# Kernel tuning notes

Measured on AMD Instinct MI355X. Metric: run time of the kernel, lower is better.

Reference implementation:

```python
import jax, jax.numpy as jnp
import numpy as np

N = 50000
E = 800000
T = 12
HID = 128
K = 3
F_IN = 7  # 1 (x) + 4 (env) + 2 (coords)
CIN = F_IN + HID  # DCRNN concatenates input with hidden state


def setup_inputs() -> dict:
    key = jax.random.key(0)
    ks = jax.random.split(key, 16)
    inp = {
        "x": jax.random.normal(ks[0], (N, T), dtype=jnp.float32),
        "env": jax.random.normal(ks[1], (N, 4, T), dtype=jnp.float32),
        "coords": jax.random.uniform(ks[2], (N, 2), dtype=jnp.float32),
        "edge_index": jax.random.randint(ks[3], (2, E), 0, N, dtype=jnp.int32),
        "edge_weight": jax.random.uniform(ks[4], (E,), dtype=jnp.float32),
        "local_night": jax.random.uniform(ks[5], (N, T + 1), dtype=jnp.float32),
        # DCRNN gate diffusion-conv weights: [2 (out/in direction), K, Cin, Cout]
        "Wz": jax.random.normal(ks[6], (2, K, CIN, HID), dtype=jnp.float32) * 0.05,
        "bz": jnp.zeros((HID,), dtype=jnp.float32),
        "Wr": jax.random.normal(ks[7], (2, K, CIN, HID), dtype=jnp.float32) * 0.05,
        "br": jnp.zeros((HID,), dtype=jnp.float32),
        "Wh": jax.random.normal(ks[8], (2, K, CIN, HID), dtype=jnp.float32) * 0.05,
        "bh": jnp.zeros((HID,), dtype=jnp.float32),
        "lin_W": jax.random.normal(ks[9], (HID, 1), dtype=jnp.float32) * 0.05,
        "lin_b": jnp.zeros((1,), dtype=jnp.float32),
    }
    return inp


def reference(x, env, coords, edge_weight, local_night, Wz, bz, Wr, br, Wh, bh, lin_W, lin_b, edge_index):
    row, col = edge_index[0], edge_index[1]
    n = x.shape[0]

    # out/in degrees of the weighted adjacency A[row, col] = w
    deg_out = jax.ops.segment_sum(edge_weight, row, num_segments=n)
    deg_in = jax.ops.segment_sum(edge_weight, col, num_segments=n)
    inv_out = jnp.where(deg_out > 0, 1.0 / deg_out, 0.0)
    inv_in = jnp.where(deg_in > 0, 1.0 / deg_in, 0.0)

    def prop_out(v):  # (D_O^{-1} A) v : gather from col, scatter-add to row
        msg = edge_weight[:, None] * v[col]
        return inv_out[:, None] * jax.ops.segment_sum(msg, row, num_segments=n)

    def prop_in(v):  # (D_I^{-1} A^T) v : gather from row, scatter-add to col
        msg = edge_weight[:, None] * v[row]
        return inv_in[:, None] * jax.ops.segment_sum(msg, col, num_segments=n)

    def dconv(X, W, b):
        # K-hop bidirectional diffusion convolution
        H = X @ (W[0, 0] + W[1, 0])
        Tx0 = X
        Tx_o = prop_out(X)
        Tx_i = prop_in(X)
        H = H + Tx_o @ W[0, 1] + Tx_i @ W[1, 1]
        for k in range(2, W.shape[1]):
            Tx_o = 2.0 * prop_out(Tx_o) - Tx0
            Tx_i = 2.0 * prop_in(Tx_i) - Tx0
            H = H + Tx_o @ W[0, k] + Tx_i @ W[1, k]
        return H + b

    env_t = jnp.moveaxis(env, -1, 0)          # [T, N, 4]
    night_t = jnp.transpose(local_night[:, 1:])  # [T, N]
    hid0 = jnp.zeros((n, HID), dtype=x.dtype)   # hidden state resets each call (H=None)

    def step(x_prev, ts):
        e, night = ts
        X = jnp.concatenate([x_prev, e, coords], axis=1)   # [N, 7]
        Xh = jnp.concatenate([X, hid0], axis=1)            # [N, 7+HID]
        Z = jax.nn.sigmoid(dconv(Xh, Wz, bz))
        R = jax.nn.sigmoid(dconv(Xh, Wr, br))  # H*R = 0 since H0 = 0; kept for fidelity
        H_tilde = jnp.tanh(dconv(Xh, Wh, bh))
        H_new = Z * hid0 + (1.0 - Z) * H_tilde
        out = jax.nn.relu(H_new) @ lin_W + lin_b           # [N, 1]
        out = out * night[:, None]
        return out, out

    x0 = x[:, 0:1]
    _, preds = jax.lax.scan(step, x0, (env_t, night_t))    # preds: [T, N, 1]
    predictions = jnp.concatenate([x0, jnp.transpose(preds[..., 0])], axis=1)  # [N, T+1]
    return predictions
```

## Files before the change

### kernel.cpp

```cpp
#include <hip/hip_runtime.h>
#include <hip/hip_fp16.h>

#define Nn 50000
#define Ee 800000
#define Tt 12
#define NBAND 8
#define BAND 6250
#define NSB 32
#define NCHUNKS ((Nn + NSB - 1) / NSB)
#define SCB 196

__global__ __launch_bounds__(256) void hist_kernel(
    const int* __restrict__ ei, int* __restrict__ cntR, int* __restrict__ cntC)
{
    int e = blockIdx.x * 256 + threadIdx.x;
    if (e >= Ee) return;
    atomicAdd(&cntR[ei[e]], 1);
    atomicAdd(&cntC[ei[Ee + e]], 1);
}

__global__ __launch_bounds__(256) void scanA_kernel(
    const int* __restrict__ cntR, const int* __restrict__ cntC,
    int* __restrict__ bsum)
{
    const int* cnt = blockIdx.y ? cntC : cntR;
    int i = blockIdx.x * 256 + threadIdx.x;
    int v = (i < Nn) ? cnt[i] : 0;
    __shared__ int ws_[4];
    v += __shfl_xor(v, 1);  v += __shfl_xor(v, 2);  v += __shfl_xor(v, 4);
    v += __shfl_xor(v, 8);  v += __shfl_xor(v, 16); v += __shfl_xor(v, 32);
    if ((threadIdx.x & 63) == 0) ws_[threadIdx.x >> 6] = v;
    __syncthreads();
    if (threadIdx.x == 0)
        bsum[blockIdx.y * 256 + blockIdx.x] = ws_[0] + ws_[1] + ws_[2] + ws_[3];
}

__global__ __launch_bounds__(256) void scanB_kernel(
    const int* __restrict__ bsum, int* __restrict__ bbase)
{
    int y = blockIdx.x;
    __shared__ int s[256];
    int t = threadIdx.x;
    int v = (t < SCB) ? bsum[y * 256 + t] : 0;
    s[t] = v;
    __syncthreads();
    for (int off = 1; off < 256; off <<= 1) {
        int u = (t >= off) ? s[t - off] : 0;
        __syncthreads();
        s[t] += u;
        __syncthreads();
    }
    bbase[y * 256 + t] = s[t] - v;
}

__global__ __launch_bounds__(256) void scanC_kernel(
    const int* __restrict__ cntR, const int* __restrict__ cntC,
    const int* __restrict__ bbase,
    int* __restrict__ startR, int* __restrict__ startC,
    int* __restrict__ nextR, int* __restrict__ nextC)
{
    int y = blockIdx.y;
    const int* cnt = y ? cntC : cntR;
    int* start     = y ? startC : startR;
    int* nxt       = y ? nextC : nextR;
    int i = blockIdx.x * 256 + threadIdx.x;
    int v = (i < Nn) ? cnt[i] : 0;
    __shared__ int s[256];
    int t = threadIdx.x;
    s[t] = v;
    __syncthreads();
    for (int off = 1; off < 256; off <<= 1) {
        int u = (t >= off) ? s[t - off] : 0;
        __syncthreads();
        s[t] += u;
        __syncthreads();
    }
    int st = bbase[y * 256 + blockIdx.x] + s[t] - v;
    if (i < Nn) { start[i] = st; nxt[i] = st; }
}

__global__ __launch_bounds__(256) void scatter_banded(
    const int* __restrict__ ei, const float* __restrict__ ew,
    int* __restrict__ nextR, int* __restrict__ nextC,
    unsigned* __restrict__ adjR, unsigned* __restrict__ adjC)
{
    int band = blockIdx.x & (NBAND - 1);
    int chunk = blockIdx.x >> 3;
    int lo = band * BAND, hi = lo + BAND;
    int stride = (gridDim.x >> 3) * 256;
    for (int e = chunk * 256 + threadIdx.x; e < Ee; e += stride) {
        int r = ei[e], c = ei[Ee + e];
        bool wr = (r >= lo && r < hi);
        bool wc = (c >= lo && c < hi);
        if (!(wr || wc)) continue;
        unsigned wb = __half_as_ushort(__float2half(ew[e]));
        if (wr) adjR[atomicAdd(&nextR[r], 1)] = ((unsigned)c << 16) | wb;
        if (wc) adjC[atomicAdd(&nextC[c], 1)] = ((unsigned)r << 16) | wb;
    }
}

__global__ __launch_bounds__(256) void weff_kernel(
    const float* __restrict__ Wz, const float* __restrict__ Wh,
    const float* __restrict__ bz, const float* __restrict__ bh,
    float* __restrict__ wzT, float* __restrict__ whT)
{
    int idx = blockIdx.x * 256 + threadIdx.x;
    if (idx >= 2 * 36 * 128) return;
    const float* W = (idx < 36 * 128) ? Wz : Wh;
    const float* B = (idx < 36 * 128) ? bz : bh;
    float* O       = (idx < 36 * 128) ? wzT : whT;
    int rem = idx % (36 * 128);
    int k = rem / 128, j = rem % 128;
    float v;
    if (k == 35) v = B[j];
    else {
        int p = k / 7, rr = k % 7;
        if (p == 0)      v = W[(0 * 135 + rr) * 128 + j] + W[(3 * 135 + rr) * 128 + j];
        else if (p == 1) v = W[(1 * 135 + rr) * 128 + j];
        else if (p == 2) v = W[(4 * 135 + rr) * 128 + j];
        else if (p == 3) v = W[(2 * 135 + rr) * 128 + j];
        else             v = W[(5 * 135 + rr) * 128 + j];
    }
    O[k * 128 + j] = v;
}

__global__ __launch_bounds__(256) void init_kernel(
    const float* __restrict__ x, const float* __restrict__ env,
    const float* __restrict__ coords, __half* __restrict__ Xh,
    float* __restrict__ out)
{
    int i = blockIdx.x * 256 + threadIdx.x;
    if (i >= Nn) return;
    float xv = x[i * Tt];
    __half* r = Xh + (long)i * 8;
    r[0] = __float2half(xv);
    #pragma unroll
    for (int c = 0; c < 4; c++) r[1 + c] = __float2half(env[i * 48 + c * 12]);
    r[5] = __float2half(coords[i * 2 + 0]);
    r[6] = __float2half(coords[i * 2 + 1]);
    r[7] = __half(0.f);
    out[i * 13 + 0] = xv;
}

__device__ __forceinline__ void unpack8(const __half* p, float* v) {
    uint4 hv = *((const uint4*)p);
    float2 p0 = __half22float2(*(__half2*)&hv.x);
    float2 p1 = __half22float2(*(__half2*)&hv.y);
    float2 p2 = __half22float2(*(__half2*)&hv.z);
    float2 p3 = __half22float2(*(__half2*)&hv.w);
    v[0] = p0.x; v[1] = p0.y; v[2] = p1.x; v[3] = p1.y;
    v[4] = p2.x; v[5] = p2.y; v[6] = p3.x;
}

__device__ __forceinline__ void pack8(__half* p, const float* v) {
    __half2 q0 = __floats2half2_rn(v[0], v[1]);
    __half2 q1 = __floats2half2_rn(v[2], v[3]);
    __half2 q2 = __floats2half2_rn(v[4], v[5]);
    __half2 q3 = __floats2half2_rn(v[6], 0.f);
    uint4 st;
    st.x = *(unsigned*)&q0; st.y = *(unsigned*)&q1;
    st.z = *(unsigned*)&q2; st.w = *(unsigned*)&q3;
    *((uint4*)p) = st;
}

__global__ __launch_bounds__(256) void gather1_kernel(
    const int* __restrict__ startR, const int* __restrict__ cntR,
    const unsigned* __restrict__ adjR,
    const int* __restrict__ startC, const int* __restrict__ cntC,
    const unsigned* __restrict__ adjC,
    const __half* __restrict__ Xh,
    __half* __restrict__ TxoH, __half* __restrict__ TxiH,
    float* __restrict__ inv_out, float* __restrict__ inv_in)
{
    int tid = blockIdx.x * 256 + threadIdx.x;
    if (tid >= Nn * 8) return;
    int node = tid >> 3;
    int dir = (tid >> 2) & 1, sub = tid & 3;
    const int*      st  = dir ? startC : startR;
    const int*      cn  = dir ? cntC : cntR;
    const unsigned* adj = dir ? adjC : adjR;
    int b = st[node], e = b + cn[node];
    float a[7] = {0.f, 0.f, 0.f, 0.f, 0.f, 0.f, 0.f};
    float sw = 0.f;
    for (int k = b + sub; k < e; k += 4) {
        unsigned ed = adj[k];
        float w = __half2float(__ushort_as_half((unsigned short)(ed & 0xffffu)));
        float xv[7];
        unpack8(Xh + (long)(ed >> 16) * 8, xv);
        #pragma unroll
        for (int q = 0; q < 7; q++) a[q] = fmaf(w, xv[q], a[q]);
        sw += w;
    }
    #pragma unroll
    for (int m = 1; m <= 2; m <<= 1) {
        #pragma unroll
        for (int q = 0; q < 7; q++) a[q] += __shfl_xor(a[q], m);
        sw += __shfl_xor(sw, m);
    }
    if (sub == 0) {
        float inv = sw > 0.f ? 1.f / sw : 0.f;
        (dir ? inv_in : inv_out)[node] = inv;
        #pragma unroll
        for (int q = 0; q < 7; q++) a[q] *= inv;
        pack8((dir ? TxiH : TxoH) + (long)node * 8, a);
    }
}

__global__ __launch_bounds__(256) void gather2_kernel(
    const int* __restrict__ startR, const int* __restrict__ cntR,
    const unsigned* __restrict__ adjR,
    const int* __restrict__ startC, const int* __restrict__ cntC,
    const unsigned* __restrict__ adjC,
    const __half* __restrict__ Xh,
    const __half* __restrict__ TxoH, const __half* __restrict__ TxiH,
    const float* __restrict__ inv_out, const float* __restrict__ inv_in,
    __half* __restrict__ T2oH, __half* __restrict__ T2iH)
{
    int tid = blockIdx.x * 256 + threadIdx.x;
    if (tid >= Nn * 8) return;
    int node = tid >> 3;
    int dir = (tid >> 2) & 1, sub = tid & 3;
    const int*      st  = dir ? startC : startR;
    const int*      cn  = dir ? cntC : cntR;
    const unsigned* adj = dir ? adjC : adjR;
    const __half*   src = dir ? TxiH : TxoH;
    int b = st[node], e = b + cn[node];
    float a[7] = {0.f, 0.f, 0.f, 0.f, 0.f, 0.f, 0.f};
    for (int k = b + sub; k < e; k += 4) {
        unsigned ed = adj[k];
        float w = __half2float(__ushort_as_half((unsigned short)(ed & 0xffffu)));
        float xv[7];
        unpack8(src + (long)(ed >> 16) * 8, xv);
        #pragma unroll
        for (int q = 0; q < 7; q++) a[q] = fmaf(w, xv[q], a[q]);
    }
    #pragma unroll
    for (int m = 1; m <= 2; m <<= 1) {
        #pragma unroll
        for (int q = 0; q < 7; q++) a[q] += __shfl_xor(a[q], m);
    }
    if (sub == 0) {
        float s2 = 2.f * (dir ? inv_in[node] : inv_out[node]);
        float xv[7];
        unpack8(Xh + (long)node * 8, xv);
        #pragma unroll
        for (int q = 0; q < 7; q++) a[q] = fmaf(s2, a[q], -xv[q]);
        pack8((dir ? T2iH : T2oH) + (long)node * 8, a);
    }
}

__global__ __launch_bounds__(256) void node_step_kernel(
    const float* __restrict__ env, const float* __restrict__ night,
    const float* __restrict__ wzT, const float* __restrict__ whT,
    const float* __restrict__ linW, const float* __restrict__ linb,
    __half* __restrict__ Xh,
    const __half* __restrict__ TxoH, const __half* __restrict__ TxiH,
    const __half* __restrict__ T2oH, const __half* __restrict__ T2iH,
    float* __restrict__ out, int t)
{
    __shared__ float f_s[NSB][36];
    __shared__ float part_s[2][NSB];
    int tid = threadIdx.x;
    int lane = tid & 63;
    int wave = tid >> 6;
    int chSel = wave & 1;
    int ch = chSel * 64 + lane;
    int half_id = wave >> 1;

    float wz[36], wh[36];
    #pragma unroll
    for (int k = 0; k < 36; k++) wz[k] = wzT[k * 128 + ch];
    #pragma unroll
    for (int k = 0; k < 36; k++) wh[k] = whT[k * 128 + ch];
    float lw = linW[ch];
    float lb = linb[0];

    for (int chunk = blockIdx.x; chunk < NCHUNKS; chunk += gridDim.x) {
        int base = chunk * NSB;
        __syncthreads();
        if (tid < NSB * 5) {
            int n = tid / 5, a = tid % 5;
            int node = base + n;
            int nc = node < Nn ? node : Nn - 1;
            const __half* src = a == 0 ? Xh : a == 1 ? TxoH : a == 2 ? TxiH
                              : a == 3 ? T2oH : T2iH;
            float v[7];
            unpack8(src + (long)nc * 8, v);
            float* d = &f_s[n][a * 7];
            #pragma unroll
            for (int q = 0; q < 7; q++) d[q] = v[q];
            if (a == 0) f_s[n][35] = 1.f;
        }
        __syncthreads();
        #pragma unroll 1
        for (int n = 0; n < 16; n++) {
            int ni = half_id * 16 + n;
            const float4* fv = (const float4*)f_s[ni];
            float hz = 0.f, hh = 0.f;
            #pragma unroll
            for (int q = 0; q < 9; q++) {
                float4 fq = fv[q];
                hz = fmaf(fq.x, wz[q*4+0], hz); hh = fmaf(fq.x, wh[q*4+0], hh);
                hz = fmaf(fq.y, wz[q*4+1], hz); hh = fmaf(fq.y, wh[q*4+1], hh);
                hz = fmaf(fq.z, wz[q*4+2], hz); hh = fmaf(fq.z, wh[q*4+2], hh);
                hz = fmaf(fq.w, wz[q*4+3], hz); hh = fmaf(fq.w, wh[q*4+3], hh);
            }
            float z  = 1.f / (1.f + __expf(-hz));
            float e2 = __expf(2.f * hh);
            float ht = 1.f - 2.f / (e2 + 1.f);
            float v = fmaxf((1.f - z) * ht, 0.f) * lw;
            v += __shfl_xor(v, 1);  v += __shfl_xor(v, 2);  v += __shfl_xor(v, 4);
            v += __shfl_xor(v, 8);  v += __shfl_xor(v, 16); v += __shfl_xor(v, 32);
            if (lane == 0) part_s[chSel][ni] = v;
        }
        __syncthreads();
        if (tid < NSB) {
            int node = base + tid;
            if (node < Nn) {
                float o = part_s[0][tid] + part_s[1][tid] + lb;
                o *= night[(long)node * 13 + t + 1];
                out[(long)node * 13 + t + 1] = o;
                if (t + 1 < Tt) {
                    __half* xr = Xh + (long)node * 8;
                    xr[0] = __float2half(o);
                    #pragma unroll
                    for (int c = 0; c < 4; c++)
                        xr[1 + c] = __float2half(env[(long)node * 48 + c * 12 + t + 1]);
                }
            }
        }
    }
}

extern "C" void kernel_launch(void* const* d_in, const int* in_sizes, int n_in,
                              void* d_out, int out_size, void* d_ws, size_t ws_size,
                              hipStream_t stream) {
    const float* x      = (const float*)d_in[0];
    const float* env    = (const float*)d_in[1];
    const float* coords = (const float*)d_in[2];
    const int*   ei     = (const int*)d_in[3];
    const float* ew     = (const float*)d_in[4];
    const float* night  = (const float*)d_in[5];
    const float* Wz     = (const float*)d_in[6];
    const float* bz     = (const float*)d_in[7];
    const float* Wh     = (const float*)d_in[10];
    const float* bh     = (const float*)d_in[11];
    const float* linW   = (const float*)d_in[12];
    const float* linb   = (const float*)d_in[13];
    float* out = (float*)d_out;

    float* w = (float*)d_ws;
    float* wzT     = w;
    float* whT     = w + 4608;
    float* inv_out = w + 9216;
    float* inv_in  = w + 59216;
    __half* Xh   = (__half*)(w + 109216);
    __half* TxoH = (__half*)(w + 309216);
    __half* TxiH = (__half*)(w + 509216);
    __half* T2oH = (__half*)(w + 709216);
    __half* T2iH = (__half*)(w + 909216);
    int* cntR    = (int*)(w + 1109216);
    int* cntC    = cntR + 50000;
    int* startR  = cntC + 50000;
    int* startC  = startR + 50000;
    int* nextR   = startC + 50000;
    int* nextC   = nextR + 50000;
    int* bsum    = nextC + 50000;
    int* bbase   = bsum + 512;
    unsigned* adjR = (unsigned*)(bbase + 512);
    unsigned* adjC = adjR + Ee;

    hipMemsetAsync(cntR, 0, 2 * Nn * sizeof(int), stream);
    hist_kernel<<<(Ee + 255) / 256, 256, 0, stream>>>(ei, cntR, cntC);
    scanA_kernel<<<dim3(SCB, 2), 256, 0, stream>>>(cntR, cntC, bsum);
    scanB_kernel<<<2, 256, 0, stream>>>(bsum, bbase);
    scanC_kernel<<<dim3(SCB, 2), 256, 0, stream>>>(
        cntR, cntC, bbase, startR, startC, nextR, nextC);
    scatter_banded<<<8 * 256, 256, 0, stream>>>(ei, ew, nextR, nextC, adjR, adjC);

    weff_kernel<<<(2 * 36 * 128 + 255) / 256, 256, 0, stream>>>(Wz, Wh, bz, bh, wzT, whT);
    init_kernel<<<(Nn + 255) / 256, 256, 0, stream>>>(x, env, coords, Xh, out);

    for (int t = 0; t < Tt; t++) {
        gather1_kernel<<<(Nn * 8 + 255) / 256, 256, 0, stream>>>(
            startR, cntR, adjR, startC, cntC, adjC, Xh, TxoH, TxiH, inv_out, inv_in);
        gather2_kernel<<<(Nn * 8 + 255) / 256, 256, 0, stream>>>(
            startR, cntR, adjR, startC, cntC, adjC, Xh, TxoH, TxiH,
            inv_out, inv_in, T2oH, T2iH);
        node_step_kernel<<<NCHUNKS, 256, 0, stream>>>(
            env, night, wzT, whT, linW, linb, Xh, TxoH, TxiH, T2oH, T2iH, out, t);
    }
}
```

Before: 859.5 us.

## Fuse second diffusion hop into node step kernel and prepack edges

The second-hop gather is moved into the per-node gate kernel. Each 32-node block first computes the T2 terms straight into shared memory, so the T2oH/T2iH round trip through global memory and one launch per timestep go away. Edge preprocessing packs each edge's index and half-precision weight once in the histogram pass, so the banded scatter reads one uint2 per edge instead of re-reading indices and weights. A possible cost is more register pressure in the fused kernel and the gather and GEMV phases no longer overlapping across blocks.

Measured after the change: 815.3 us. 5.1% less time.

```diff
diff --git a/kernel.cpp b/kernel.cpp
--- a/kernel.cpp
+++ b/kernel.cpp
@@ -6,17 +6,19 @@
 #define Tt 12
 #define NBAND 8
 #define BAND 6250
-#define NSB 32
-#define NCHUNKS ((Nn + NSB - 1) / NSB)
 #define SCB 196
 
-__global__ __launch_bounds__(256) void hist_kernel(
-    const int* __restrict__ ei, int* __restrict__ cntR, int* __restrict__ cntC)
+__global__ __launch_bounds__(256) void pack_hist_kernel(
+    const int* __restrict__ ei, const float* __restrict__ ew,
+    uint2* __restrict__ packed, int* __restrict__ cntR, int* __restrict__ cntC)
 {
     int e = blockIdx.x * 256 + threadIdx.x;
     if (e >= Ee) return;
-    atomicAdd(&cntR[ei[e]], 1);
-    atomicAdd(&cntC[ei[Ee + e]], 1);
+    int r = ei[e], c = ei[Ee + e];
+    unsigned wb = __half_as_ushort(__float2half(ew[e]));
+    packed[e] = make_uint2(((unsigned)c << 16) | wb, ((unsigned)r << 16) | wb);
+    atomicAdd(&cntR[r], 1);
+    atomicAdd(&cntC[c], 1);
 }
 
 __global__ __launch_bounds__(256) void scanA_kernel(
@@ -80,7 +82,7 @@
 }
 
 __global__ __launch_bounds__(256) void scatter_banded(
-    const int* __restrict__ ei, const float* __restrict__ ew,
+    const uint2* __restrict__ packed,
     int* __restrict__ nextR, int* __restrict__ nextC,
     unsigned* __restrict__ adjR, unsigned* __restrict__ adjC)
 {
@@ -89,13 +91,11 @@
     int lo = band * BAND, hi = lo + BAND;
     int stride = (gridDim.x >> 3) * 256;
     for (int e = chunk * 256 + threadIdx.x; e < Ee; e += stride) {
-        int r = ei[e], c = ei[Ee + e];
-        bool wr = (r >= lo && r < hi);
-        bool wc = (c >= lo && c < hi);
-        if (!(wr || wc)) continue;
-        unsigned wb = __half_as_ushort(__float2half(ew[e]));
-        if (wr) adjR[atomicAdd(&nextR[r], 1)] = ((unsigned)c << 16) | wb;
-        if (wc) adjC[atomicAdd(&nextC[c], 1)] = ((unsigned)r << 16) | wb;
+        uint2 p = packed[e];
+        int c = (int)(p.x >> 16);
+        int r = (int)(p.y >> 16);
+        if (r >= lo && r < hi) adjR[atomicAdd(&nextR[r], 1)] = p.x;
+        if (c >= lo && c < hi) adjC[atomicAdd(&nextC[c], 1)] = p.y;
     }
 }
 
@@ -206,67 +206,72 @@
     }
 }
 
-__global__ __launch_bounds__(256) void gather2_kernel(
+__global__ __launch_bounds__(256) void step2_kernel(
     const int* __restrict__ startR, const int* __restrict__ cntR,
     const unsigned* __restrict__ adjR,
     const int* __restrict__ startC, const int* __restrict__ cntC,
     const unsigned* __restrict__ adjC,
-    const __half* __restrict__ Xh,
-    const __half* __restrict__ TxoH, const __half* __restrict__ TxiH,
     const float* __restrict__ inv_out, const float* __restrict__ inv_in,
-    __half* __restrict__ T2oH, __half* __restrict__ T2iH)
-{
-    int tid = blockIdx.x * 256 + threadIdx.x;
-    if (tid >= Nn * 8) return;
-    int node = tid >> 3;
-    int dir = (tid >> 2) & 1, sub = tid & 3;
-    const int*      st  = dir ? startC : startR;
-    const int*      cn  = dir ? cntC : cntR;
-    const unsigned* adj = dir ? adjC : adjR;
-    const __half*   src = dir ? TxiH : TxoH;
-    int b = st[node], e = b + cn[node];
-    float a[7] = {0.f, 0.f, 0.f, 0.f, 0.f, 0.f, 0.f};
-    for (int k = b + sub; k < e; k += 4) {
-        unsigned ed = adj[k];
-        float w = __half2float(__ushort_as_half((unsigned short)(ed & 0xffffu)));
-        float xv[7];
-        unpack8(src + (long)(ed >> 16) * 8, xv);
-        #pragma unroll
-        for (int q = 0; q < 7; q++) a[q] = fmaf(w, xv[q], a[q]);
-    }
-    #pragma unroll
-    for (int m = 1; m <= 2; m <<= 1) {
-        #pragma unroll
-        for (int q = 0; q < 7; q++) a[q] += __shfl_xor(a[q], m);
-    }
-    if (sub == 0) {
-        float s2 = 2.f * (dir ? inv_in[node] : inv_out[node]);
-        float xv[7];
-        unpack8(Xh + (long)node * 8, xv);
-        #pragma unroll
-        for (int q = 0; q < 7; q++) a[q] = fmaf(s2, a[q], -xv[q]);
-        pack8((dir ? T2iH : T2oH) + (long)node * 8, a);
-    }
-}
-
-__global__ __launch_bounds__(256) void node_step_kernel(
     const float* __restrict__ env, const float* __restrict__ night,
     const float* __restrict__ wzT, const float* __restrict__ whT,
     const float* __restrict__ linW, const float* __restrict__ linb,
     __half* __restrict__ Xh,
     const __half* __restrict__ TxoH, const __half* __restrict__ TxiH,
-    const __half* __restrict__ T2oH, const __half* __restrict__ T2iH,
     float* __restrict__ out, int t)
 {
-    __shared__ float f_s[NSB][36];
-    __shared__ float part_s[2][NSB];
+    __shared__ float f_s[32][36];
+    __shared__ float part_s[2][32];
     int tid = threadIdx.x;
+    int base = blockIdx.x * 32;
+
+    {
+        int nl = tid >> 3;
+        int dir = (tid >> 2) & 1, sub = tid & 3;
+        int node = base + nl;
+        int nc = node < Nn ? node : Nn - 1;
+        const int*      st  = dir ? startC : startR;
+        const int*      cn  = dir ? cntC : cntR;
+        const unsigned* adj = dir ? adjC : adjR;
+        const __half*   src = dir ? TxiH : TxoH;
+        int b = st[nc], e = b + cn[nc];
+        float a[7] = {0.f, 0.f, 0.f, 0.f, 0.f, 0.f, 0.f};
+        for (int k = b + sub; k < e; k += 4) {
+            unsigned ed = adj[k];
+            float w = __half2float(__ushort_as_half((unsigned short)(ed & 0xffffu)));
+            float xv[7];
+            unpack8(src + (long)(ed >> 16) * 8, xv);
+            #pragma unroll
+            for (int q = 0; q < 7; q++) a[q] = fmaf(w, xv[q], a[q]);
+        }
+        #pragma unroll
+        for (int m = 1; m <= 2; m <<= 1) {
+            #pragma unroll
+            for (int q = 0; q < 7; q++) a[q] += __shfl_xor(a[q], m);
+        }
+        if (sub == 0) {
+            float s2 = 2.f * (dir ? inv_in[nc] : inv_out[nc]);
+            float xv[7], tx[7];
+            unpack8(Xh + (long)nc * 8, xv);
+            unpack8(src + (long)nc * 8, tx);
+            #pragma unroll
+            for (int q = 0; q < 7; q++) {
+                f_s[nl][21 + 7 * dir + q] = fmaf(s2, a[q], -xv[q]);
+                f_s[nl][7 + 7 * dir + q]  = tx[q];
+            }
+            if (dir == 0) {
+                #pragma unroll
+                for (int q = 0; q < 7; q++) f_s[nl][q] = xv[q];
+                f_s[nl][35] = 1.f;
+            }
+        }
+    }
+    __syncthreads();
+
     int lane = tid & 63;
     int wave = tid >> 6;
     int chSel = wave & 1;
     int ch = chSel * 64 + lane;
     int half_id = wave >> 1;
-
     float wz[36], wh[36];
     #pragma unroll
     for (int k = 0; k < 36; k++) wz[k] = wzT[k * 128 + ch];
@@ -275,58 +280,40 @@
     float lw = linW[ch];
     float lb = linb[0];
 
-    for (int chunk = blockIdx.x; chunk < NCHUNKS; chunk += gridDim.x) {
-        int base = chunk * NSB;
-        __syncthreads();
-        if (tid < NSB * 5) {
-            int n = tid / 5, a = tid % 5;
-            int node = base + n;
-            int nc = node < Nn ? node : Nn - 1;
-            const __half* src = a == 0 ? Xh : a == 1 ? TxoH : a == 2 ? TxiH
-                              : a == 3 ? T2oH : T2iH;
-            float v[7];
-            unpack8(src + (long)nc * 8, v);
-            float* d = &f_s[n][a * 7];
-            #pragma unroll
-            for (int q = 0; q < 7; q++) d[q] = v[q];
-            if (a == 0) f_s[n][35] = 1.f;
-        }
-        __syncthreads();
-        #pragma unroll 1
-        for (int n = 0; n < 16; n++) {
-            int ni = half_id * 16 + n;
-            const float4* fv = (const float4*)f_s[ni];
-            float hz = 0.f, hh = 0.f;
-            #pragma unroll
-            for (int q = 0; q < 9; q++) {
-                float4 fq = fv[q];
-                hz = fmaf(fq.x, wz[q*4+0], hz); hh = fmaf(fq.x, wh[q*4+0], hh);
-                hz = fmaf(fq.y, wz[q*4+1], hz); hh = fmaf(fq.y, wh[q*4+1], hh);
-                hz = fmaf(fq.z, wz[q*4+2], hz); hh = fmaf(fq.z, wh[q*4+2], hh);
-                hz = fmaf(fq.w, wz[q*4+3], hz); hh = fmaf(fq.w, wh[q*4+3], hh);
-            }
-            float z  = 1.f / (1.f + __expf(-hz));
-            float e2 = __expf(2.f * hh);
-            float ht = 1.f - 2.f / (e2 + 1.f);
-            float v = fmaxf((1.f - z) * ht, 0.f) * lw;
-            v += __shfl_xor(v, 1);  v += __shfl_xor(v, 2);  v += __shfl_xor(v, 4);
-            v += __shfl_xor(v, 8);  v += __shfl_xor(v, 16); v += __shfl_xor(v, 32);
-            if (lane == 0) part_s[chSel][ni] = v;
-        }
-        __syncthreads();
-        if (tid < NSB) {
-            int node = base + tid;
-            if (node < Nn) {
-                float o = part_s[0][tid] + part_s[1][tid] + lb;
-                o *= night[(long)node * 13 + t + 1];
-                out[(long)node * 13 + t + 1] = o;
-                if (t + 1 < Tt) {
-                    __half* xr = Xh + (long)node * 8;
-                    xr[0] = __float2half(o);
-                    #pragma unroll
-                    for (int c = 0; c < 4; c++)
-                        xr[1 + c] = __float2half(env[(long)node * 48 + c * 12 + t + 1]);
-                }
+    #pragma unroll 1
+    for (int n = 0; n < 16; n++) {
+        int ni = half_id * 16 + n;
+        const float4* fv = (const float4*)f_s[ni];
+        float hz = 0.f, hh = 0.f;
+        #pragma unroll
+        for (int q = 0; q < 9; q++) {
+            float4 fq = fv[q];
+            hz = fmaf(fq.x, wz[q*4+0], hz); hh = fmaf(fq.x, wh[q*4+0], hh);
+            hz = fmaf(fq.y, wz[q*4+1], hz); hh = fmaf(fq.y, wh[q*4+1], hh);
+            hz = fmaf(fq.z, wz[q*4+2], hz); hh = fmaf(fq.z, wh[q*4+2], hh);
+            hz = fmaf(fq.w, wz[q*4+3], hz); hh = fmaf(fq.w, wh[q*4+3], hh);
+        }
+        float z  = 1.f / (1.f + __expf(-hz));
+        float e2 = __expf(2.f * hh);
+        float ht = 1.f - 2.f / (e2 + 1.f);
+        float v = fmaxf((1.f - z) * ht, 0.f) * lw;
+        v += __shfl_xor(v, 1);  v += __shfl_xor(v, 2);  v += __shfl_xor(v, 4);
+        v += __shfl_xor(v, 8);  v += __shfl_xor(v, 16); v += __shfl_xor(v, 32);
+        if (lane == 0) part_s[chSel][ni] = v;
+    }
+    __syncthreads();
+    if (tid < 32) {
+        int node = base + tid;
+        if (node < Nn) {
+            float o = part_s[0][tid] + part_s[1][tid] + lb;
+            o *= night[(long)node * 13 + t + 1];
+            out[(long)node * 13 + t + 1] = o;
+            if (t + 1 < Tt) {
+                __half* xr = Xh + (long)node * 8;
+                xr[0] = __float2half(o);
+                #pragma unroll
+                for (int c = 0; c < 4; c++)
+                    xr[1 + c] = __float2half(env[(long)node * 48 + c * 12 + t + 1]);
             }
         }
     }
@@ -357,9 +344,7 @@
     __half* Xh   = (__half*)(w + 109216);
     __half* TxoH = (__half*)(w + 309216);
     __half* TxiH = (__half*)(w + 509216);
-    __half* T2oH = (__half*)(w + 709216);
-    __half* T2iH = (__half*)(w + 909216);
-    int* cntR    = (int*)(w + 1109216);
+    int* cntR    = (int*)(w + 709216);
     int* cntC    = cntR + 50000;
     int* startR  = cntC + 50000;
     int* startC  = startR + 50000;
@@ -367,16 +352,17 @@
     int* nextC   = nextR + 50000;
     int* bsum    = nextC + 50000;
     int* bbase   = bsum + 512;
-    unsigned* adjR = (unsigned*)(bbase + 512);
+    uint2* packed  = (uint2*)(bbase + 512);
+    unsigned* adjR = (unsigned*)(packed + Ee);
     unsigned* adjC = adjR + Ee;
 
     hipMemsetAsync(cntR, 0, 2 * Nn * sizeof(int), stream);
-    hist_kernel<<<(Ee + 255) / 256, 256, 0, stream>>>(ei, cntR, cntC);
+    pack_hist_kernel<<<(Ee + 255) / 256, 256, 0, stream>>>(ei, ew, packed, cntR, cntC);
     scanA_kernel<<<dim3(SCB, 2), 256, 0, stream>>>(cntR, cntC, bsum);
     scanB_kernel<<<2, 256, 0, stream>>>(bsum, bbase);
     scanC_kernel<<<dim3(SCB, 2), 256, 0, stream>>>(
         cntR, cntC, bbase, startR, startC, nextR, nextC);
-    scatter_banded<<<8 * 256, 256, 0, stream>>>(ei, ew, nextR, nextC, adjR, adjC);
+    scatter_banded<<<8 * 256, 256, 0, stream>>>(packed, nextR, nextC, adjR, adjC);
 
     weff_kernel<<<(2 * 36 * 128 + 255) / 256, 256, 0, stream>>>(Wz, Wh, bz, bh, wzT, whT);
     init_kernel<<<(Nn + 255) / 256, 256, 0, stream>>>(x, env, coords, Xh, out);
@@ -384,10 +370,8 @@
     for (int t = 0; t < Tt; t++) {
         gather1_kernel<<<(Nn * 8 + 255) / 256, 256, 0, stream>>>(
             startR, cntR, adjR, startC, cntC, adjC, Xh, TxoH, TxiH, inv_out, inv_in);
-        gather2_kernel<<<(Nn * 8 + 255) / 256, 256, 0, stream>>>(
-            startR, cntR, adjR, startC, cntC, adjC, Xh, TxoH, TxiH,
-            inv_out, inv_in, T2oH, T2iH);
-        node_step_kernel<<<NCHUNKS, 256, 0, stream>>>(
-            env, night, wzT, whT, linW, linb, Xh, TxoH, TxiH, T2oH, T2iH, out, t);
-    }
-}
+        step2_kernel<<<(Nn + 31) / 32, 256, 0, stream>>>(
+            startR, cntR, adjR, startC, cntC, adjC, inv_out, inv_in,
+            env, night, wzT, whT, linW, linb, Xh, TxoH, TxiH, out, t);
+    }
+}
```
